# Performance work log

Measured on AMD Instinct MI355X. Metric: run time of the kernel, lower is better.

The kernel has to match this reference:

```python
import jax, jax.numpy as jnp
import numpy as np

RES = 16          # grid resolution per axis -> num_models = 4096
L_XYZ = 10        # xyz positional-encoding frequencies -> input_ch = 63
L_DIR = 4         # dir positional-encoding frequencies -> input_ch_views = 27
W = 32
N_RAYS, N_SAMPLES = 1024, 128
NM = RES * RES * RES


def _embed(x, L):
    # NeRF frequency encoding: [x, sin(2^k x), cos(2^k x)] for k in 0..L-1
    freqs = 2.0 ** jnp.arange(L, dtype=x.dtype)          # (L,)
    xf = x[..., None, :] * freqs[:, None]                # (N, L, 3)
    enc = jnp.concatenate([jnp.sin(xf), jnp.cos(xf)], axis=-1)
    return jnp.concatenate([x, enc.reshape(x.shape[0], -1)], axis=-1)


def setup_inputs() -> dict:
    key = jax.random.key(0)
    ks = jax.random.split(key, 16)
    s = 0.05
    pts = jax.random.uniform(ks[0], (N_RAYS, N_SAMPLES, 3), dtype=jnp.float32)
    vd = jax.random.normal(ks[1], (N_RAYS, 3), dtype=jnp.float32)
    vd = vd / jnp.linalg.norm(vd, axis=-1, keepdims=True)
    return {
        "pts": pts,
        "viewdirs": vd,
        "pts_w0": s * jax.random.normal(ks[2], (NM, W, 63), dtype=jnp.float32),
        "pts_b0": s * jax.random.normal(ks[3], (NM, W), dtype=jnp.float32),
        "pts_w1": s * jax.random.normal(ks[4], (NM, W, W), dtype=jnp.float32),
        "pts_b1": s * jax.random.normal(ks[5], (NM, W), dtype=jnp.float32),
        "feat_w": s * jax.random.normal(ks[6], (NM, W, W), dtype=jnp.float32),
        "feat_b": s * jax.random.normal(ks[7], (NM, W), dtype=jnp.float32),
        "sigma_w": s * jax.random.normal(ks[8], (NM, 1, W), dtype=jnp.float32),
        "sigma_b": s * jax.random.normal(ks[9], (NM, 1), dtype=jnp.float32),
        "view_w": s * jax.random.normal(ks[10], (NM, W, W + 27), dtype=jnp.float32),
        "view_b": s * jax.random.normal(ks[11], (NM, W), dtype=jnp.float32),
        "rgb_w": s * jax.random.normal(ks[12], (NM, 3, W), dtype=jnp.float32),
        "rgb_b": s * jax.random.normal(ks[13], (NM, 3), dtype=jnp.float32),
    }


def reference(pts, viewdirs, pts_w0, pts_b0, pts_w1, pts_b1, feat_w, feat_b,
              sigma_w, sigma_b, view_w, view_b, rgb_w, rgb_b):
    n_rays, n_samples, _ = pts.shape
    p = pts.reshape(-1, 3)                                        # (N, 3)
    v = jnp.broadcast_to(viewdirs[:, None, :],
                         (n_rays, n_samples, 3)).reshape(-1, 3)   # (N, 3)

    # voxel index (aabb = [0,1]^3)
    scaled = jnp.clip(p * RES, 0.0, RES - 1.0)
    i3 = scaled.astype(jnp.int32)
    idx = i3[:, 0] * (RES * RES) + i3[:, 1] * RES + i3[:, 2]      # (N,)

    ep = _embed(p, L_XYZ)                                         # (N, 63)
    ev = _embed(v, L_DIR)                                         # (N, 27)

    # per-point tiny MLP with gathered weights: h @ w^T + b
    h = jax.nn.relu(jnp.einsum('nd,nod->no', ep, pts_w0[idx]) + pts_b0[idx])
    h = jax.nn.relu(jnp.einsum('nd,nod->no', h, pts_w1[idx]) + pts_b1[idx])

    sigma = jnp.einsum('nd,nod->no', h, sigma_w[idx]) + sigma_b[idx]   # (N, 1)
    feat = jnp.einsum('nd,nod->no', h, feat_w[idx]) + feat_b[idx]      # (N, W)

    h2 = jnp.concatenate([feat, ev], axis=-1)                          # (N, W+27)
    h2 = jax.nn.relu(jnp.einsum('nd,nod->no', h2, view_w[idx]) + view_b[idx])
    rgb = jnp.einsum('nd,nod->no', h2, rgb_w[idx]) + rgb_b[idx]        # (N, 3)

    out = jnp.concatenate([rgb, sigma], axis=-1).reshape(n_rays, n_samples, 4)
    return out[..., :3], out[..., 3:4]
```

## Files before the change

kernel.cpp:

```cpp
#include <hip/hip_runtime.h>

#define NM    4096
#define NPTS  131072
#define CAP   128

typedef _Float16 h8 __attribute__((ext_vector_type(8)));
typedef _Float16 h2 __attribute__((ext_vector_type(2)));
typedef float    f4 __attribute__((ext_vector_type(4)));
typedef int      i4 __attribute__((ext_vector_type(4)));

#define MF(a, b, c) __builtin_amdgcn_mfma_f32_16x16x32_f16((a), (b), (c), 0, 0, 0)

static __device__ inline h2 pk(float a, float b) {
    return __builtin_bit_cast(h2, __builtin_amdgcn_cvt_pkrtz(a, b));
}

static __device__ inline h8 pack8(float u0, float u1, float u2, float u3,
                                  float u4, float u5, float u6, float u7) {
    i4 t;
    t[0] = __builtin_bit_cast(int, pk(u0, u1));
    t[1] = __builtin_bit_cast(int, pk(u2, u3));
    t[2] = __builtin_bit_cast(int, pk(u4, u5));
    t[3] = __builtin_bit_cast(int, pk(u6, u7));
    return __builtin_bit_cast(h8, t);
}

static __device__ inline h8 load_row8(const float* __restrict__ rb, int d0, int lim) {
    float u[8];
    #pragma unroll
    for (int jj = 0; jj < 8; jj++) {
        int d = d0 + jj;
        u[jj] = (d < lim) ? rb[d] : 0.f;
    }
    return pack8(u[0], u[1], u[2], u[3], u[4], u[5], u[6], u[7]);
}

static __device__ inline float encdim(int d, int lim, float x, float y, float z) {
    int tt = d - 3;
    int k  = tt / 6;
    int r  = tt - 6 * k;
    float p = x;
    p = (r == 1 || r == 4) ? y : p;
    p = (r == 2 || r == 5) ? z : p;
    float f   = __int_as_float((k + 127) << 23);
    float arg = p * f + ((r >= 3) ? 1.57079632679f : 0.f);
    float sv  = __sinf(arg);
    float raw = (d == 0) ? x : ((d == 1) ? y : z);
    float val = (d < 3) ? raw : sv;
    return (d < lim) ? val : 0.f;
}

static __device__ inline h8 makeB(f4 d0, f4 d1, int quad, int col) {
    int laneA = ((quad & 1) * 2) * 16 + col;
    int laneB = laneA + 16;
    float a0 = __shfl(d0[0], laneA), b0 = __shfl(d1[0], laneA);
    float a1 = __shfl(d0[1], laneA), b1 = __shfl(d1[1], laneA);
    float a2 = __shfl(d0[2], laneA), b2 = __shfl(d1[2], laneA);
    float a3 = __shfl(d0[3], laneA), b3 = __shfl(d1[3], laneA);
    float a4 = __shfl(d0[0], laneB), b4 = __shfl(d1[0], laneB);
    float a5 = __shfl(d0[1], laneB), b5 = __shfl(d1[1], laneB);
    float a6 = __shfl(d0[2], laneB), b6 = __shfl(d1[2], laneB);
    float a7 = __shfl(d0[3], laneB), b7 = __shfl(d1[3], laneB);
    bool hi = quad >= 2;
    return pack8(hi ? b0 : a0, hi ? b1 : a1, hi ? b2 : a2, hi ? b3 : a3,
                 hi ? b4 : a4, hi ? b5 : a5, hi ? b6 : a6, hi ? b7 : a7);
}

static __device__ inline f4 relu4(f4 a) {
    f4 r;
    r[0] = fmaxf(a[0], 0.f); r[1] = fmaxf(a[1], 0.f);
    r[2] = fmaxf(a[2], 0.f); r[3] = fmaxf(a[3], 0.f);
    return r;
}

__global__ __launch_bounds__(256) void k_bucket(const float* __restrict__ pts,
                                                int* __restrict__ count,
                                                int* __restrict__ plist) {
    int n = blockIdx.x * 256 + threadIdx.x;
    if (n >= NPTS) return;
    float x = pts[3 * n + 0], y = pts[3 * n + 1], z = pts[3 * n + 2];
    int ix = (int)fminf(fmaxf(x * 16.f, 0.f), 15.f);
    int iy = (int)fminf(fmaxf(y * 16.f, 0.f), 15.f);
    int iz = (int)fminf(fmaxf(z * 16.f, 0.f), 15.f);
    int v = (ix << 8) | (iy << 4) | iz;
    int pos = atomicAdd(&count[v], 1);
    if (pos < CAP) plist[v * CAP + pos] = n;
}

__global__ __launch_bounds__(64) void k_mlp(
    const float* __restrict__ pts, const float* __restrict__ vds,
    const float* __restrict__ w0g, const float* __restrict__ b0g,
    const float* __restrict__ w1g, const float* __restrict__ b1g,
    const float* __restrict__ fwg, const float* __restrict__ fbg,
    const float* __restrict__ swg, const float* __restrict__ sbg,
    const float* __restrict__ vwg, const float* __restrict__ vbg,
    const float* __restrict__ rwg, const float* __restrict__ rbg,
    const int* __restrict__ count, const int* __restrict__ plist,
    float* __restrict__ out) {
    const int v = blockIdx.x;
    const int t = threadIdx.x;
    const int c = min(count[v], CAP);
    if (c == 0) return;

    const int col  = t & 15;
    const int quad = t >> 4;
    const int k8   = quad * 8;

    float pxc, pyc, pzc, dxc, dyc, dzc;
    int ncur;
    {
        int sl = min(col, c - 1);
        ncur = plist[v * CAP + sl];
        pxc = pts[3 * ncur]; pyc = pts[3 * ncur + 1]; pzc = pts[3 * ncur + 2];
        int ray = ncur >> 7;
        dxc = vds[3 * ray]; dyc = vds[3 * ray + 1]; dzc = vds[3 * ray + 2];
    }

    h8 aW0[2][2], aVW[2][2], aW1[2], aFW[2];
    #pragma unroll
    for (int Ti = 0; Ti < 2; Ti++) {
        const float* rb = w0g + (size_t)v * 2016 + (Ti * 16 + col) * 63;
        aW0[Ti][0] = load_row8(rb, k8, 63);
        aW0[Ti][1] = load_row8(rb, 32 + k8, 63);
        rb = vwg + (size_t)v * 1888 + (Ti * 16 + col) * 59;
        aVW[Ti][0] = load_row8(rb, k8, 59);
        aVW[Ti][1] = load_row8(rb, 32 + k8, 59);
        rb = w1g + (size_t)v * 1024 + (Ti * 16 + col) * 32;
        aW1[Ti] = load_row8(rb, k8, 32);
        rb = fwg + (size_t)v * 1024 + (Ti * 16 + col) * 32;
        aFW[Ti] = load_row8(rb, k8, 32);
    }
    h8 aSG = {};
    if (col == 0) aSG = load_row8(swg + (size_t)v * 32, k8, 32);
    h8 aRGB = {};
    if (col < 3) aRGB = load_row8(rwg + (size_t)v * 96 + col * 32, k8, 32);

    f4 cB0[2], cB1[2], cFB[2], cVB[2];
    #pragma unroll
    for (int Ti = 0; Ti < 2; Ti++) {
        #pragma unroll
        for (int r = 0; r < 4; r++) {
            int row = Ti * 16 + quad * 4 + r;
            cB0[Ti][r] = b0g[v * 32 + row];
            cB1[Ti][r] = b1g[v * 32 + row];
            cFB[Ti][r] = fbg[v * 32 + row];
            cVB[Ti][r] = vbg[v * 32 + row];
        }
    }
    const float rb0 = rbg[v * 3 + 0], rb1 = rbg[v * 3 + 1], rb2 = rbg[v * 3 + 2];
    const float sb  = sbg[v];
    const f4 z4 = {0.f, 0.f, 0.f, 0.f};

    for (int base = 0; base < c; base += 16) {
        const bool active = (base + col) < c;
        const int n = ncur;
        const float px = pxc, py = pyc, pz = pzc;
        const float dx = dxc, dy = dyc, dz = dzc;

        if (base + 16 < c) {
            int sl = min(base + 16 + col, c - 1);
            ncur = plist[v * CAP + sl];
            pxc = pts[3 * ncur]; pyc = pts[3 * ncur + 1]; pzc = pts[3 * ncur + 2];
            int ray = ncur >> 7;
            dxc = vds[3 * ray]; dyc = vds[3 * ray + 1]; dzc = vds[3 * ray + 2];
        }

        h8 bE0 = pack8(encdim(k8 + 0, 63, px, py, pz), encdim(k8 + 1, 63, px, py, pz),
                       encdim(k8 + 2, 63, px, py, pz), encdim(k8 + 3, 63, px, py, pz),
                       encdim(k8 + 4, 63, px, py, pz), encdim(k8 + 5, 63, px, py, pz),
                       encdim(k8 + 6, 63, px, py, pz), encdim(k8 + 7, 63, px, py, pz));
        h8 bE1 = pack8(encdim(32 + k8 + 0, 63, px, py, pz), encdim(32 + k8 + 1, 63, px, py, pz),
                       encdim(32 + k8 + 2, 63, px, py, pz), encdim(32 + k8 + 3, 63, px, py, pz),
                       encdim(32 + k8 + 4, 63, px, py, pz), encdim(32 + k8 + 5, 63, px, py, pz),
                       encdim(32 + k8 + 6, 63, px, py, pz), encdim(32 + k8 + 7, 63, px, py, pz));

        f4 d0 = MF(aW0[0][0], bE0, cB0[0]); d0 = MF(aW0[0][1], bE1, d0);
        f4 d1 = MF(aW0[1][0], bE0, cB0[1]); d1 = MF(aW0[1][1], bE1, d1);
        d0 = relu4(d0); d1 = relu4(d1);
        h8 bH = makeB(d0, d1, quad, col);

        f4 e0 = MF(aW1[0], bH, cB1[0]);
        f4 e1 = MF(aW1[1], bH, cB1[1]);
        e0 = relu4(e0); e1 = relu4(e1);
        h8 bG = makeB(e0, e1, quad, col);

        f4 s = MF(aSG, bG, z4);

        f4 f0 = MF(aFW[0], bG, cFB[0]);
        f4 f1 = MF(aFW[1], bG, cFB[1]);
        h8 bF = makeB(f0, f1, quad, col);

        h8 bD = pack8(encdim(k8 + 0, 27, dx, dy, dz), encdim(k8 + 1, 27, dx, dy, dz),
                      encdim(k8 + 2, 27, dx, dy, dz), encdim(k8 + 3, 27, dx, dy, dz),
                      encdim(k8 + 4, 27, dx, dy, dz), encdim(k8 + 5, 27, dx, dy, dz),
                      encdim(k8 + 6, 27, dx, dy, dz), encdim(k8 + 7, 27, dx, dy, dz));

        f4 v0 = MF(aVW[0][0], bF, cVB[0]); v0 = MF(aVW[0][1], bD, v0);
        f4 v1 = MF(aVW[1][0], bF, cVB[1]); v1 = MF(aVW[1][1], bD, v1);
        v0 = relu4(v0); v1 = relu4(v1);
        h8 bV = makeB(v0, v1, quad, col);

        f4 o = MF(aRGB, bV, z4);

        if (quad == 0 && active) {
            out[3 * n + 0] = o[0] + rb0;
            out[3 * n + 1] = o[1] + rb1;
            out[3 * n + 2] = o[2] + rb2;
            out[3 * NPTS + n] = s[0] + sb;
        }
    }
}

extern "C" void kernel_launch(void* const* d_in, const int* in_sizes, int n_in,
                              void* d_out, int out_size, void* d_ws, size_t ws_size,
                              hipStream_t stream) {
    const float* pts = (const float*)d_in[0];
    const float* vds = (const float*)d_in[1];
    const float* w0  = (const float*)d_in[2];
    const float* b0  = (const float*)d_in[3];
    const float* w1  = (const float*)d_in[4];
    const float* b1  = (const float*)d_in[5];
    const float* fw  = (const float*)d_in[6];
    const float* fb  = (const float*)d_in[7];
    const float* sw  = (const float*)d_in[8];
    const float* sb  = (const float*)d_in[9];
    const float* vw  = (const float*)d_in[10];
    const float* vb  = (const float*)d_in[11];
    const float* rw  = (const float*)d_in[12];
    const float* rb  = (const float*)d_in[13];
    float* out = (float*)d_out;

    int* count = (int*)d_ws;
    int* plist = (int*)((char*)d_ws + NM * sizeof(int));

    (void)hipMemsetAsync(count, 0, NM * sizeof(int), stream);
    k_bucket<<<NPTS / 256, 256, 0, stream>>>(pts, count, plist);
    k_mlp<<<NM, 64, 0, stream>>>(pts, vds, w0, b0, w1, b1, fw, fb, sw, sb,
                                 vw, vb, rw, rb, count, plist, out);
}
```

Baseline: 182.9 us.

## Stage per-voxel weights through LDS using global_load_lds DMA

Weight matrices for each voxel's MLP are now copied into shared memory with coalesced 16-byte global_load_lds transfers in two phases (w0/w1, then view/feat/sigma/rgb). Each thread then builds its MFMA fragments from LDS. Previously it issued strided scalar global loads per row. The goal is to turn uncoalesced row-wise global reads into contiguous bulk copies, at the cost of extra barriers and LDS use per block. A fallback keeps the old path when the builtin is missing.

Measured after the change: 167.8 us. -8.3%, faster.

```diff
diff --git a/kernel.cpp b/kernel.cpp
--- a/kernel.cpp
+++ b/kernel.cpp
@@ -10,6 +10,12 @@
 typedef int      i4 __attribute__((ext_vector_type(4)));
 
 #define MF(a, b, c) __builtin_amdgcn_mfma_f32_16x16x32_f16((a), (b), (c), 0, 0, 0)
+
+#if __has_builtin(__builtin_amdgcn_global_load_lds)
+#define USE_DMA 1
+#else
+#define USE_DMA 0
+#endif
 
 static __device__ inline h2 pk(float a, float b) {
     return __builtin_bit_cast(h2, __builtin_amdgcn_cvt_pkrtz(a, b));
@@ -23,6 +29,24 @@
     t[2] = __builtin_bit_cast(int, pk(u4, u5));
     t[3] = __builtin_bit_cast(int, pk(u6, u7));
     return __builtin_bit_cast(h8, t);
+}
+
+static __device__ inline h8 lds_row8(const float* __restrict__ X, int base,
+                                     int d0, int lim) {
+    float u[8];
+    #pragma unroll
+    for (int jj = 0; jj < 8; jj++) {
+        int d = d0 + jj;
+        float raw = X[base + d];
+        u[jj] = (d < lim) ? raw : 0.f;
+    }
+    return pack8(u[0], u[1], u[2], u[3], u[4], u[5], u[6], u[7]);
+}
+
+static __device__ inline h8 lds_row8a(const float* __restrict__ X, int off) {
+    f4 v0 = *(const f4*)(X + off);
+    f4 v1 = *(const f4*)(X + off + 4);
+    return pack8(v0[0], v0[1], v0[2], v0[3], v1[0], v1[1], v1[2], v1[3]);
 }
 
 static __device__ inline h8 load_row8(const float* __restrict__ rb, int d0, int lim) {
@@ -73,6 +97,14 @@
     return r;
 }
 
+#if USE_DMA
+static __device__ inline void dma16(const float* g, const float* l) {
+    __builtin_amdgcn_global_load_lds(
+        (const __attribute__((address_space(1))) void*)g,
+        (__attribute__((address_space(3))) void*)l, 16, 0, 0);
+}
+#endif
+
 __global__ __launch_bounds__(256) void k_bucket(const float* __restrict__ pts,
                                                 int* __restrict__ count,
                                                 int* __restrict__ plist) {
@@ -97,6 +129,8 @@
     const float* __restrict__ rwg, const float* __restrict__ rbg,
     const int* __restrict__ count, const int* __restrict__ plist,
     float* __restrict__ out) {
+    __shared__ __align__(16) float X[3040];
+
     const int v = blockIdx.x;
     const int t = threadIdx.x;
     const int c = min(count[v], CAP);
@@ -105,6 +139,18 @@
     const int col  = t & 15;
     const int quad = t >> 4;
     const int k8   = quad * 8;
+
+#if USE_DMA
+    {
+        const float* g = w0g + (size_t)v * 2016;
+        #pragma unroll
+        for (int k = 0; k < 7; k++) dma16(g + k * 256 + t * 4, X + k * 256);
+        if (t < 56) dma16(g + 1792 + t * 4, X + 1792);
+        g = w1g + (size_t)v * 1024;
+        #pragma unroll
+        for (int k = 0; k < 4; k++) dma16(g + k * 256 + t * 4, X + 2016 + k * 256);
+    }
+#endif
 
     float pxc, pyc, pzc, dxc, dyc, dzc;
     int ncur;
@@ -115,8 +161,58 @@
         int ray = ncur >> 7;
         dxc = vds[3 * ray]; dyc = vds[3 * ray + 1]; dzc = vds[3 * ray + 2];
     }
-
-    h8 aW0[2][2], aVW[2][2], aW1[2], aFW[2];
+    f4 cB0[2], cB1[2], cFB[2], cVB[2];
+    #pragma unroll
+    for (int Ti = 0; Ti < 2; Ti++) {
+        #pragma unroll
+        for (int r = 0; r < 4; r++) {
+            int row = Ti * 16 + quad * 4 + r;
+            cB0[Ti][r] = b0g[v * 32 + row];
+            cB1[Ti][r] = b1g[v * 32 + row];
+            cFB[Ti][r] = fbg[v * 32 + row];
+            cVB[Ti][r] = vbg[v * 32 + row];
+        }
+    }
+    const float rb0 = rbg[v * 3 + 0], rb1 = rbg[v * 3 + 1], rb2 = rbg[v * 3 + 2];
+    const float sb  = sbg[v];
+
+    h8 aW0[2][2], aVW[2][2], aW1[2], aFW[2], aSG, aRGB;
+
+#if USE_DMA
+    __syncthreads();
+
+    #pragma unroll
+    for (int Ti = 0; Ti < 2; Ti++) {
+        int rbase = (Ti * 16 + col) * 63;
+        aW0[Ti][0] = lds_row8(X, rbase, k8, 63);
+        aW0[Ti][1] = lds_row8(X, rbase, 32 + k8, 63);
+        aW1[Ti] = lds_row8a(X, 2016 + (Ti * 16 + col) * 32 + k8);
+    }
+    __syncthreads();
+
+    {
+        const float* g = vwg + (size_t)v * 1888;
+        #pragma unroll
+        for (int k = 0; k < 7; k++) dma16(g + k * 256 + t * 4, X + k * 256);
+        if (t < 24) dma16(g + 1792 + t * 4, X + 1792);
+        g = fwg + (size_t)v * 1024;
+        #pragma unroll
+        for (int k = 0; k < 4; k++) dma16(g + k * 256 + t * 4, X + 1888 + k * 256);
+        if (t < 8)  dma16(swg + (size_t)v * 32 + t * 4, X + 2912);
+        if (t < 24) dma16(rwg + (size_t)v * 96 + t * 4, X + 2944);
+    }
+    __syncthreads();
+
+    #pragma unroll
+    for (int Ti = 0; Ti < 2; Ti++) {
+        int rbase = (Ti * 16 + col) * 59;
+        aVW[Ti][0] = lds_row8(X, rbase, k8, 59);
+        aVW[Ti][1] = lds_row8(X, rbase, 32 + k8, 59);
+        aFW[Ti] = lds_row8a(X, 1888 + (Ti * 16 + col) * 32 + k8);
+    }
+    aSG = (col == 0) ? lds_row8a(X, 2912 + k8) : h8{};
+    aRGB = (col < 3) ? lds_row8a(X, 2944 + col * 32 + k8) : h8{};
+#else
     #pragma unroll
     for (int Ti = 0; Ti < 2; Ti++) {
         const float* rb = w0g + (size_t)v * 2016 + (Ti * 16 + col) * 63;
@@ -125,30 +221,13 @@
         rb = vwg + (size_t)v * 1888 + (Ti * 16 + col) * 59;
         aVW[Ti][0] = load_row8(rb, k8, 59);
         aVW[Ti][1] = load_row8(rb, 32 + k8, 59);
-        rb = w1g + (size_t)v * 1024 + (Ti * 16 + col) * 32;
-        aW1[Ti] = load_row8(rb, k8, 32);
-        rb = fwg + (size_t)v * 1024 + (Ti * 16 + col) * 32;
-        aFW[Ti] = load_row8(rb, k8, 32);
-    }
-    h8 aSG = {};
-    if (col == 0) aSG = load_row8(swg + (size_t)v * 32, k8, 32);
-    h8 aRGB = {};
-    if (col < 3) aRGB = load_row8(rwg + (size_t)v * 96 + col * 32, k8, 32);
-
-    f4 cB0[2], cB1[2], cFB[2], cVB[2];
-    #pragma unroll
-    for (int Ti = 0; Ti < 2; Ti++) {
-        #pragma unroll
-        for (int r = 0; r < 4; r++) {
-            int row = Ti * 16 + quad * 4 + r;
-            cB0[Ti][r] = b0g[v * 32 + row];
-            cB1[Ti][r] = b1g[v * 32 + row];
-            cFB[Ti][r] = fbg[v * 32 + row];
-            cVB[Ti][r] = vbg[v * 32 + row];
-        }
-    }
-    const float rb0 = rbg[v * 3 + 0], rb1 = rbg[v * 3 + 1], rb2 = rbg[v * 3 + 2];
-    const float sb  = sbg[v];
+        aW1[Ti] = load_row8(w1g + (size_t)v * 1024 + (Ti * 16 + col) * 32, k8, 32);
+        aFW[Ti] = load_row8(fwg + (size_t)v * 1024 + (Ti * 16 + col) * 32, k8, 32);
+    }
+    aSG = (col == 0) ? load_row8(swg + (size_t)v * 32, k8, 32) : h8{};
+    aRGB = (col < 3) ? load_row8(rwg + (size_t)v * 96 + col * 32, k8, 32) : h8{};
+#endif
+
     const f4 z4 = {0.f, 0.f, 0.f, 0.f};
 
     for (int base = 0; base < c; base += 16) {
```
